# Optimization experiments

Measured on AMD Instinct MI355X. Metric: run time of the kernel, lower is better.

Reference implementation:

```python
import jax, jax.numpy as jnp
import numpy as np

NUM_HEADS = 12
DIM = 768
HEAD_DIM = DIM // NUM_HEADS
NUM_BUCKETS = 32
MAX_DISTANCE = 128
ELEV_SCALE = 1000.0


def _bucket_positions(relative_position):
    # Faithful port of RelativePositionBias2D._bucket_positions (torch .long() truncates;
    # values passed through the large branch are non-negative so astype(int32) matches).
    nb = NUM_BUCKETS // 2  # 16
    n = -relative_position
    ret = (n < 0).astype(jnp.int32) * nb
    n = jnp.abs(n)
    max_exact = nb // 2  # 8
    is_small = n < max_exact
    n_safe = jnp.maximum(n, 1).astype(jnp.float32)  # avoid log(0); masked by is_small
    val_if_large = max_exact + (
        jnp.log(n_safe / max_exact) / np.float32(np.log(MAX_DISTANCE / max_exact)) * (nb - max_exact)
    ).astype(jnp.int32)
    val_if_large = jnp.minimum(val_if_large, nb - 1)
    return ret + jnp.where(is_small, n, val_if_large)


def _bucket_idx(coords_2d):
    # coords_2d: [B, N, 2] in [0,1] -> integer grid coords
    coords_int = (coords_2d * MAX_DISTANCE).astype(jnp.int32)
    rel_x = coords_int[:, :, None, 0] - coords_int[:, None, :, 0]  # [B,N,N]
    rel_y = coords_int[:, :, None, 1] - coords_int[:, None, :, 1]
    bx = _bucket_positions(rel_x)
    by = _bucket_positions(rel_y)
    return bx * NUM_BUCKETS + by  # [B,N,N] int32 in [0, 1024)


def setup_inputs() -> dict:
    key = jax.random.key(0)
    ks = jax.random.split(key, 8)
    B, N, D = 4, 1024, DIM
    x = jax.random.normal(ks[0], (B, N, D), dtype=jnp.float32)
    coords_2d = jax.random.uniform(ks[1], (B, N, 2), dtype=jnp.float32)
    elevation_patches = jax.random.normal(ks[2], (B, N), dtype=jnp.float32) * 2000.0  # meters
    qkv_w = jax.random.normal(ks[3], (3 * D, D), dtype=jnp.float32) * 0.02
    qkv_b = jnp.zeros((3 * D,), dtype=jnp.float32)
    proj_w = jax.random.normal(ks[4], (D, D), dtype=jnp.float32) * 0.02
    proj_b = jnp.zeros((D,), dtype=jnp.float32)
    bias_table = jax.random.normal(ks[5], (NUM_BUCKETS * NUM_BUCKETS, NUM_HEADS), dtype=jnp.float32) * 0.02
    alpha = jnp.full((1,), 2.0, dtype=jnp.float32)
    return {"x": x, "coords_2d": coords_2d, "elevation_patches": elevation_patches,
            "qkv_w": qkv_w, "qkv_b": qkv_b, "proj_w": proj_w, "proj_b": proj_b,
            "bias_table": bias_table, "alpha": alpha}


def reference(x, coords_2d, elevation_patches, qkv_w, qkv_b, proj_w, proj_b, bias_table, alpha):
    B, N, D = x.shape
    H, hd = NUM_HEADS, HEAD_DIM
    scale = hd ** -0.5

    qkv = x @ qkv_w.T + qkv_b  # [B,N,3D]
    qkv = qkv.reshape(B, N, 3, H, hd)
    q = qkv[:, :, 0].transpose(0, 2, 1, 3)  # [B,H,N,hd]
    k = qkv[:, :, 1].transpose(0, 2, 1, 3)
    v = qkv[:, :, 2].transpose(0, 2, 1, 3)

    attn = jnp.einsum('bhnd,bhmd->bhnm', q * scale, k)  # [B,H,N,N]

    # relative position bias: gather from table, [B,N,N,H] -> [B,H,N,N]
    idx = _bucket_idx(coords_2d)
    rel_bias = bias_table[idx].transpose(0, 3, 1, 2)
    attn = attn + rel_bias

    # elevation bias: [B,N,N], broadcast over heads
    elev_diff = (elevation_patches[:, None, :] - elevation_patches[:, :, None]) / ELEV_SCALE
    elev_bias = jnp.clip(-alpha[0] * jax.nn.relu(elev_diff), -10.0, 0.0)
    attn = attn + elev_bias[:, None, :, :]

    attn = jax.nn.softmax(attn.astype(jnp.float32), axis=-1).astype(q.dtype)

    out = jnp.einsum('bhnm,bhmd->bhnd', attn, v)  # [B,H,N,hd]
    out = out.transpose(0, 2, 1, 3).reshape(B, N, D)
    return out @ proj_w.T + proj_b
```

## Files before the change

kernel.cpp:

```cpp
#include <hip/hip_runtime.h>
#include <hip/hip_bf16.h>
#include <math.h>

#define NH 12
#define HD 64
#define NSEQ 1024
#define DMODEL 768
#define LOG2E 1.44269504f

typedef unsigned short ushort_t;
typedef float f32x4 __attribute__((ext_vector_type(4)));
typedef short bf16x8 __attribute__((ext_vector_type(8)));

__device__ __forceinline__ ushort_t f2bf(float f) {
    unsigned int u = __float_as_uint(f);
    u += 0x7FFFu + ((u >> 16) & 1u);
    return (ushort_t)(u >> 16);
}

__device__ __forceinline__ unsigned pk2(float x, float y) {
    __hip_bfloat162 t = __float22bfloat162_rn(make_float2(x, y));
    union { __hip_bfloat162 b; unsigned u; } c; c.b = t;
    return c.u;
}

__device__ __forceinline__ void gl_lds16(const ushort_t* g, ushort_t* l) {
    __builtin_amdgcn_global_load_lds(
        (const __attribute__((address_space(1))) unsigned int*)g,
        (__attribute__((address_space(3))) unsigned int*)l, 16, 0, 0);
}

#define XB_N   3145728u
#define WQB_N  1769472u
#define PWB_N  589824u
#define CVT_BLOCKS 2400

__global__ __launch_bounds__(256) void prep_kernel(
    const float* __restrict__ x, const float* __restrict__ w1,
    ushort_t* __restrict__ dst)
{
    const int t = threadIdx.x;
    const unsigned i = blockIdx.x * 256 + t;
    const unsigned n0 = XB_N / 8, n1 = n0 + WQB_N / 8;
    if (i >= n1) return;
    const float* src; unsigned off;
    if (i < n0) { src = x;  off = i; }
    else        { src = w1; off = i - n0; }
    const float4 a = ((const float4*)src)[off * 2];
    const float4 b = ((const float4*)src)[off * 2 + 1];
    uint4 pk;
    pk.x = pk2(a.x, a.y); pk.y = pk2(a.z, a.w);
    pk.z = pk2(b.x, b.y); pk.w = pk2(b.z, b.w);
    ((uint4*)dst)[i] = pk;
}

__device__ __forceinline__ int bucketf(int rel) {
    const int n = -rel;
    const int u = (n < 0) ? 16 : 0;
    const int a = n < 0 ? -n : n;
    if (a < 8) return u + a;
    int v = 8 + (int)(log2f((float)a * 0.125f) * 2.0f + 1e-4f);
    if (v > 15) v = 15;
    return u + v;
}

#define QKV_BLOCKS 576
#define PACK_BLOCKS 4096
#define PW_BLOCKS 288

__global__ __launch_bounds__(256) void qkv_gemm(
    const ushort_t* __restrict__ A, const ushort_t* __restrict__ B,
    const float* __restrict__ bias,
    ushort_t* __restrict__ Qb, ushort_t* __restrict__ Kb, ushort_t* __restrict__ Vtb,
    const float* __restrict__ coords, const float* __restrict__ elev,
    const float* __restrict__ alpha_p, unsigned* __restrict__ pack,
    const float* __restrict__ pw, ushort_t* __restrict__ pwb)
{
    __shared__ __align__(16) ushort_t SM[32768];
    const int t = threadIdx.x;

    if (blockIdx.x >= QKV_BLOCKS + PACK_BLOCKS) {
        const unsigned i = (blockIdx.x - QKV_BLOCKS - PACK_BLOCKS) * 256 + t;
        if (i >= PWB_N / 8) return;
        const float4 a = ((const float4*)pw)[i * 2];
        const float4 b = ((const float4*)pw)[i * 2 + 1];
        uint4 pk;
        pk.x = pk2(a.x, a.y); pk.y = pk2(a.z, a.w);
        pk.z = pk2(b.x, b.y); pk.w = pk2(b.z, b.w);
        ((uint4*)pwb)[i] = pk;
        return;
    }
    if (blockIdx.x >= QKV_BLOCKS) {
        const int blk = blockIdx.x - QKV_BLOCKS;
        const int b = blk >> 10, i = blk & 1023;
        const float alpha = alpha_p[0];
        const float2 ci = *(const float2*)&coords[(size_t)(b * NSEQ + i) * 2];
        const int cxi = (int)(ci.x * 128.0f), cyi = (int)(ci.y * 128.0f);
        const float ei = elev[b * NSEQ + i];
        const int j0 = t * 4;
        const float4 c01 = *(const float4*)&coords[(size_t)(b * NSEQ + j0) * 2];
        const float4 c23 = *(const float4*)&coords[(size_t)(b * NSEQ + j0 + 2) * 2];
        const float4 ej4 = *(const float4*)&elev[b * NSEQ + j0];
        const float cjx[4] = {c01.x, c01.z, c23.x, c23.z};
        const float cjy[4] = {c01.y, c01.w, c23.y, c23.w};
        const float ejv[4] = {ej4.x, ej4.y, ej4.z, ej4.w};
        unsigned r[4];
        #pragma unroll
        for (int k = 0; k < 4; ++k) {
            const int bx = bucketf(cxi - (int)(cjx[k] * 128.0f));
            const int by = bucketf(cyi - (int)(cjy[k] * 128.0f));
            const int idx = (bx << 5) + by;
            const float ed = (ejv[k] - ei) * 1e-3f;
            const float eb = fmaxf(-alpha * fmaxf(ed, 0.0f), -10.0f) * LOG2E;
            r[k] = ((unsigned)f2bf(eb) << 16) | (unsigned)idx;
        }
        uint4 o; o.x = r[0]; o.y = r[1]; o.z = r[2]; o.w = r[3];
        *(uint4*)&pack[((size_t)b << 20) + (size_t)i * NSEQ + j0] = o;
        return;
    }

    const int lid = (blockIdx.x & 7) * 72 + (blockIdx.x >> 3);
    const int bx = lid % 18, by = lid / 18;
    const int m0 = by * 128, c0 = bx * 128;

    const int lane = t & 63, w = t >> 6;
    const int wr = w >> 1, wc = w & 1;
    const int col = lane & 15, quad = lane >> 4;
    const int c7 = col & 7;

    const f32x4 zero = {0.f, 0.f, 0.f, 0.f};
    f32x4 acc[4][4];
    #pragma unroll
    for (int i = 0; i < 4; ++i)
        #pragma unroll
        for (int j = 0; j < 4; ++j) acc[i][j] = zero;

    const int r8 = lane >> 3, g8 = lane & 7;
    const int gsw = ((g8 ^ r8) * 8);
    const ushort_t* Ag = A + (size_t)(m0 + w * 32 + r8) * DMODEL + gsw;
    const ushort_t* Bg = B + (size_t)(c0 + w * 32 + r8) * DMODEL + gsw;
    const int wso = (w * 32) * 64;

    auto STAGE = [&](int bo, int k0) {
        ushort_t* Aw = SM + bo + wso;
        ushort_t* Bw = SM + bo + 8192 + wso;
        gl_lds16(Ag + k0, Aw);
        gl_lds16(Ag + (size_t)8 * DMODEL + k0, Aw + 8 * 64);
        gl_lds16(Ag + (size_t)16 * DMODEL + k0, Aw + 16 * 64);
        gl_lds16(Ag + (size_t)24 * DMODEL + k0, Aw + 24 * 64);
        gl_lds16(Bg + k0, Bw);
        gl_lds16(Bg + (size_t)8 * DMODEL + k0, Bw + 8 * 64);
        gl_lds16(Bg + (size_t)16 * DMODEL + k0, Bw + 16 * 64);
        gl_lds16(Bg + (size_t)24 * DMODEL + k0, Bw + 24 * 64);
    };

    STAGE(0, 0);
    __syncthreads();

    #pragma unroll 2
    for (int k = 0; k < 12; ++k) {
        const int bo = (k & 1) * 16384;
        if (k < 11) STAGE(16384 - bo, (k + 1) * 64);
        #pragma unroll
        for (int kk = 0; kk < 2; ++kk) {
            bf16x8 af[4], bf[4];
            #pragma unroll
            for (int im = 0; im < 4; ++im)
                af[im] = *(const bf16x8*)&SM[bo + (wr * 64 + im * 16 + col) * 64
                        + ((4 * kk + quad) ^ c7) * 8];
            #pragma unroll
            for (int jn = 0; jn < 4; ++jn)
                bf[jn] = *(const bf16x8*)&SM[bo + 8192 + (wc * 64 + jn * 16 + col) * 64
                        + ((4 * kk + quad) ^ c7) * 8];
            #pragma unroll
            for (int im = 0; im < 4; ++im)
                #pragma unroll
                for (int jn = 0; jn < 4; ++jn)
                    acc[im][jn] = __builtin_amdgcn_mfma_f32_16x16x32_bf16(af[im], bf[jn], acc[im][jn], 0, 0, 0);
        }
        __syncthreads();
    }

    const int cbw = c0 + wc * 64;
    const int s = cbw / DMODEL;
    const int h = (cbw % DMODEL) >> 6;
    const int b = m0 >> 10;
    const int bh = b * NH + h;
    const int n0 = (m0 & (NSEQ - 1)) + wr * 64;

    float bv[4];
    #pragma unroll
    for (int jn = 0; jn < 4; ++jn) bv[jn] = bias[cbw + jn * 16 + col];

    if (s < 2) {
        ushort_t* lt = SM + w * 1152;
        ushort_t* dst = (s == 0) ? Qb : Kb;
        const float sc = (s == 0) ? 0.125f * LOG2E : 1.0f;
        const int row16 = lane >> 2, seg = lane & 3;
        #pragma unroll
        for (int im = 0; im < 4; ++im) {
            #pragma unroll
            for (int jn = 0; jn < 4; ++jn) {
                const f32x4 a = acc[im][jn];
                #pragma unroll
                for (int r = 0; r < 4; ++r)
                    lt[(quad * 4 + r) * 72 + jn * 16 + col] = f2bf((a[r] + bv[jn]) * sc);
            }
            const uint4 u0 = *(const uint4*)&lt[row16 * 72 + seg * 8];
            const uint4 u1 = *(const uint4*)&lt[row16 * 72 + 32 + seg * 8];
            const size_t gb = ((size_t)bh * NSEQ + n0 + im * 16 + row16) * HD
                            + seg * 8;
            *(uint4*)&dst[gb] = u0;
            *(uint4*)&dst[gb + 32] = u1;
        }
    } else {
        #pragma unroll
        for (int im = 0; im < 4; ++im) {
            #pragma unroll
            for (int jn = 0; jn < 4; ++jn) {
                const int d = jn * 16 + col;
                const float bvv = bv[jn];
                const f32x4 a = acc[im][jn];
                uint2 p;
                p.x = pk2(a[0] + bvv, a[1] + bvv);
                p.y = pk2(a[2] + bvv, a[3] + bvv);
                *(uint2*)&Vtb[((size_t)bh * HD + d) * NSEQ + n0 + im * 16 + quad * 4] = p;
            }
        }
    }
}

#define RBIAS(u) (__uint_as_float((unsigned)tabu[(u) & 1023u] << 16) \
                + __uint_as_float((u) & 0xFFFF0000u))

__global__ __launch_bounds__(256) void attn_mfma(
    const ushort_t* __restrict__ Qb, const ushort_t* __restrict__ Kb,
    const ushort_t* __restrict__ Vtb,
    const unsigned* __restrict__ pack,
    const float* __restrict__ table,
    ushort_t* __restrict__ Ob)
{
    __shared__ __align__(16) ushort_t Ks[2][64 * 72];
    __shared__ __align__(16) ushort_t Vt[2][64 * 72];
    __shared__ __align__(16) ushort_t Ps[64 * 72];
    __shared__ ushort_t tabu[1024];

    const int t = threadIdx.x;
    const int lane = t & 63, w = t >> 6;
    const int col = lane & 15, quad = lane >> 4;
    const int bid = (blockIdx.x & 7) * 96 + (blockIdx.x >> 3);
    const int it = bid & 15, bh = bid >> 4;
    const int h = bh % NH, b = bh / NH;
    const int i0 = it * 64;

    for (int i = t; i < 1024; i += 256)
        tabu[i] = f2bf(table[i * NH + h] * LOG2E);

    const ushort_t* Qg = Qb + ((size_t)bh * NSEQ + i0 + w * 16 + col) * HD;
    const bf16x8 aq0 = *(const bf16x8*)(Qg + quad * 8);
    const bf16x8 aq1 = *(const bf16x8*)(Qg + 32 + quad * 8);

    const size_t kvbase = (size_t)bh * NSEQ * HD;
    const unsigned* prow = pack + ((size_t)b << 20)
                         + (size_t)(i0 + w * 16 + col) * NSEQ + quad * 4;

    const int srow = t >> 3, sc8 = (t & 7) * 8;
    const int so0 = srow * 72 + sc8;
    const int so1 = (srow + 32) * 72 + sc8;

    uint4 k0 = *(const uint4*)&Kb[kvbase + (size_t)srow * HD + sc8];
    uint4 k1 = *(const uint4*)&Kb[kvbase + (size_t)(srow + 32) * HD + sc8];
    uint4 v0 = *(const uint4*)&Vtb[kvbase + (size_t)srow * NSEQ + sc8];
    uint4 v1 = *(const uint4*)&Vtb[kvbase + (size_t)(srow + 32) * NSEQ + sc8];
    *(uint4*)&Ks[0][so0] = k0;
    *(uint4*)&Ks[0][so1] = k1;
    *(uint4*)&Vt[0][so0] = v0;
    *(uint4*)&Vt[0][so1] = v1;
    k0 = *(const uint4*)&Kb[kvbase + (size_t)(64 + srow) * HD + sc8];
    k1 = *(const uint4*)&Kb[kvbase + (size_t)(64 + srow + 32) * HD + sc8];
    v0 = *(const uint4*)&Vtb[kvbase + (size_t)srow * NSEQ + 64 + sc8];
    v1 = *(const uint4*)&Vtb[kvbase + (size_t)(srow + 32) * NSEQ + 64 + sc8];

    uint4 pk4g[4], pk4l[4];
    #pragma unroll
    for (int jb = 0; jb < 4; ++jb)
        pk4g[jb] = *(const uint4*)(prow + jb * 16);

    __syncthreads();

    float rbc[4][4], rbn[4][4];
    #pragma unroll
    for (int jb = 0; jb < 4; ++jb) {
        const uint4 pkv = pk4g[jb];
        rbc[jb][0] = RBIAS(pkv.x);
        rbc[jb][1] = RBIAS(pkv.y);
        rbc[jb][2] = RBIAS(pkv.z);
        rbc[jb][3] = RBIAS(pkv.w);
    }
    #pragma unroll
    for (int jb = 0; jb < 4; ++jb)
        pk4g[jb] = *(const uint4*)(prow + 64 + jb * 16);

    const f32x4 zero = {0.f, 0.f, 0.f, 0.f};
    f32x4 o_acc[4];
    #pragma unroll
    for (int i = 0; i < 4; ++i) o_acc[i] = zero;
    float l_l = 0.f;

    #pragma unroll 2
    for (int jt = 0; jt < 16; ++jt) {
        __syncthreads();
        const int cur = jt & 1;

        if (jt < 15) {
            *(uint4*)&Ks[cur ^ 1][so0] = k0;
            *(uint4*)&Ks[cur ^ 1][so1] = k1;
            *(uint4*)&Vt[cur ^ 1][so0] = v0;
            *(uint4*)&Vt[cur ^ 1][so1] = v1;
        }
        if (jt < 14) {
            const int j2 = (jt + 2) * 64;
            k0 = *(const uint4*)&Kb[kvbase + (size_t)(j2 + srow) * HD + sc8];
            k1 = *(const uint4*)&Kb[kvbase + (size_t)(j2 + srow + 32) * HD + sc8];
            v0 = *(const uint4*)&Vtb[kvbase + (size_t)srow * NSEQ + j2 + sc8];
            v1 = *(const uint4*)&Vtb[kvbase + (size_t)(srow + 32) * NSEQ + j2 + sc8];
            #pragma unroll
            for (int jb = 0; jb < 4; ++jb)
                pk4l[jb] = *(const uint4*)(prow + j2 + jb * 16);
        }

        f32x4 sacc[4];
        __builtin_amdgcn_s_setprio(1);
        #pragma unroll
        for (int jb = 0; jb < 4; ++jb) {
            sacc[jb] = zero;
            const bf16x8 kb0 = *(const bf16x8*)&Ks[cur][(jb * 16 + col) * 72 + quad * 8];
            const bf16x8 kb1 = *(const bf16x8*)&Ks[cur][(jb * 16 + col) * 72 + 32 + quad * 8];
            sacc[jb] = __builtin_amdgcn_mfma_f32_16x16x32_bf16(kb0, aq0, sacc[jb], 0, 0, 0);
            sacc[jb] = __builtin_amdgcn_mfma_f32_16x16x32_bf16(kb1, aq1, sacc[jb], 0, 0, 0);
        }
        __builtin_amdgcn_s_setprio(0);

        float psum = 0.f;
        #pragma unroll
        for (int jb = 0; jb < 4; ++jb) {
            const float p0 = exp2f(sacc[jb][0] + rbc[jb][0]);
            const float p1 = exp2f(sacc[jb][1] + rbc[jb][1]);
            const float p2 = exp2f(sacc[jb][2] + rbc[jb][2]);
            const float p3 = exp2f(sacc[jb][3] + rbc[jb][3]);
            psum += (p0 + p1) + (p2 + p3);
            uint2 st;
            st.x = pk2(p0, p1);
            st.y = pk2(p2, p3);
            *(uint2*)&Ps[(w * 16 + col) * 72 + jb * 16 + quad * 4] = st;
        }
        l_l += psum;

        const bf16x8 ap0 = *(const bf16x8*)&Ps[(w * 16 + col) * 72 + quad * 8];
        const bf16x8 ap1 = *(const bf16x8*)&Ps[(w * 16 + col) * 72 + 32 + quad * 8];
        __builtin_amdgcn_s_setprio(1);
        #pragma unroll
        for (int db = 0; db < 4; ++db) {
            const bf16x8 vv0 = *(const bf16x8*)&Vt[cur][(db * 16 + col) * 72 + quad * 8];
            const bf16x8 vv1 = *(const bf16x8*)&Vt[cur][(db * 16 + col) * 72 + 32 + quad * 8];
            o_acc[db] = __builtin_amdgcn_mfma_f32_16x16x32_bf16(ap0, vv0, o_acc[db], 0, 0, 0);
            o_acc[db] = __builtin_amdgcn_mfma_f32_16x16x32_bf16(ap1, vv1, o_acc[db], 0, 0, 0);
            if (jt < 15) {
                const uint4 pkv = pk4g[db];
                rbn[db][0] = RBIAS(pkv.x);
                rbn[db][1] = RBIAS(pkv.y);
                rbn[db][2] = RBIAS(pkv.z);
                rbn[db][3] = RBIAS(pkv.w);
            }
        }
        __builtin_amdgcn_s_setprio(0);

        #pragma unroll
        for (int jb = 0; jb < 4; ++jb) {
            pk4g[jb] = pk4l[jb];
            rbc[jb][0] = rbn[jb][0];
            rbc[jb][1] = rbn[jb][1];
            rbc[jb][2] = rbn[jb][2];
            rbc[jb][3] = rbn[jb][3];
        }
    }

    float l = l_l;
    l += __shfl_xor(l, 16);
    l += __shfl_xor(l, 32);
    #pragma unroll
    for (int r = 0; r < 4; ++r) {
        const float lr = __shfl(l, w * 16 + quad * 4 + r);
        const float inv = 1.f / lr;
        const int ri = w * 16 + quad * 4 + r;
        const size_t base = ((size_t)(b * NSEQ) + i0 + ri) * DMODEL + h * HD;
        #pragma unroll
        for (int db = 0; db < 4; ++db)
            Ob[base + db * 16 + col] = f2bf(o_acc[db][r] * inv);
    }
}

__global__ __launch_bounds__(256) void proj_gemm(
    const ushort_t* __restrict__ A, const ushort_t* __restrict__ B,
    const float* __restrict__ bias, float* __restrict__ out)
{
    __shared__ __align__(16) ushort_t SM[16384];
    const int t = threadIdx.x;
    const int lane = t & 63, w = t >> 6;
    const int wr = w >> 1, wc = w & 1;
    const int col = lane & 15, quad = lane >> 4;
    const int c7 = col & 7;
    const int m0 = blockIdx.y * 64, c0 = blockIdx.x * 64;

    const f32x4 zero = {0.f, 0.f, 0.f, 0.f};
    f32x4 acc[2][2];
    #pragma unroll
    for (int i = 0; i < 2; ++i)
        #pragma unroll
        for (int j = 0; j < 2; ++j) acc[i][j] = zero;

    const int r8 = lane >> 3, g8 = lane & 7;
    const int gsw = ((g8 ^ r8) * 8);
    const ushort_t* Ag = A + (size_t)(m0 + w * 16 + r8) * DMODEL + gsw;
    const ushort_t* Bg = B + (size_t)(c0 + w * 16 + r8) * DMODEL + gsw;
    const int wso = (w * 16) * 64;

    auto STAGE = [&](int bo, int k0) {
        ushort_t* Aw = SM + bo + wso;
        ushort_t* Bw = SM + bo + 4096 + wso;
        gl_lds16(Ag + k0, Aw);
        gl_lds16(Ag + (size_t)8 * DMODEL + k0, Aw + 8 * 64);
        gl_lds16(Bg + k0, Bw);
        gl_lds16(Bg + (size_t)8 * DMODEL + k0, Bw + 8 * 64);
    };

    STAGE(0, 0);
    __syncthreads();

    #pragma unroll 2
    for (int k = 0; k < 12; ++k) {
        const int bo = (k & 1) * 8192;
        if (k < 11) STAGE(8192 - bo, (k + 1) * 64);
        #pragma unroll
        for (int kk = 0; kk < 2; ++kk) {
            bf16x8 af[2], bf[2];
            #pragma unroll
            for (int im = 0; im < 2; ++im)
                af[im] = *(const bf16x8*)&SM[bo + (wr * 32 + im * 16 + col) * 64
                        + ((4 * kk + quad) ^ c7) * 8];
            #pragma unroll
            for (int jn = 0; jn < 2; ++jn)
                bf[jn] = *(const bf16x8*)&SM[bo + 4096 + (wc * 32 + jn * 16 + col) * 64
                        + ((4 * kk + quad) ^ c7) * 8];
            #pragma unroll
            for (int im = 0; im < 2; ++im)
                #pragma unroll
                for (int jn = 0; jn < 2; ++jn)
                    acc[im][jn] = __builtin_amdgcn_mfma_f32_16x16x32_bf16(af[im], bf[jn], acc[im][jn], 0, 0, 0);
        }
        __syncthreads();
    }

    #pragma unroll
    for (int im = 0; im < 2; ++im) {
        #pragma unroll
        for (int jn = 0; jn < 2; ++jn) {
            const int c = c0 + wc * 32 + jn * 16 + col;
            const float bv = bias[c];
            #pragma unroll
            for (int r = 0; r < 4; ++r) {
                const int m = m0 + wr * 32 + im * 16 + quad * 4 + r;
                out[(size_t)m * DMODEL + c] = acc[im][jn][r] + bv;
            }
        }
    }
}

extern "C" void kernel_launch(void* const* d_in, const int* in_sizes, int n_in,
                              void* d_out, int out_size, void* d_ws, size_t ws_size,
                              hipStream_t stream) {
    const float* x       = (const float*)d_in[0];
    const float* coords  = (const float*)d_in[1];
    const float* elev    = (const float*)d_in[2];
    const float* qkv_w   = (const float*)d_in[3];
    const float* qkv_b   = (const float*)d_in[4];
    const float* proj_w  = (const float*)d_in[5];
    const float* proj_b  = (const float*)d_in[6];
    const float* btable  = (const float*)d_in[7];
    const float* alpha   = (const float*)d_in[8];
    float* out = (float*)d_out;

    ushort_t* wsu = (ushort_t*)d_ws;
    ushort_t* xb  = wsu;
    ushort_t* wqb = wsu + 3145728;
    ushort_t* pwb = wsu + 4915200;
    ushort_t* Qb  = wsu + 5505024;
    ushort_t* Kb  = wsu + 8650752;
    ushort_t* Vtb = wsu + 11796480;
    ushort_t* Ob  = wsu + 14942208;
    unsigned* pck = (unsigned*)(wsu + 18087936);

    prep_kernel<<<CVT_BLOCKS, 256, 0, stream>>>(x, qkv_w, wsu);
    qkv_gemm<<<QKV_BLOCKS + PACK_BLOCKS + PW_BLOCKS, 256, 0, stream>>>(
        xb, wqb, qkv_b, Qb, Kb, Vtb, coords, elev, alpha, pck, proj_w, pwb);
    attn_mfma<<<768, 256, 0, stream>>>(Qb, Kb, Vtb, pck, btable, Ob);
    proj_gemm<<<dim3(12, 64), 256, 0, stream>>>(Ob, pwb, proj_b, out);
}
```

Before: 168.3 us.

## Move bias packing and proj weight conversion into prep kernel, use bucket LUT

Moves the relative-position/elevation pack blocks and the proj_w bf16 conversion out of the QKV GEMM launch and into the prep kernel, so the GEMM kernel only launches its 576 tile blocks. The GEMM no longer carries the large shared-memory footprint for thousands of non-GEMM blocks. The bucket function is replaced by a 257-entry shared-memory lookup table per block, avoiding log2 per element. The cost is a block-level sync and LUT build in each pack block, and a bigger prep kernel that sits serially ahead of the GEMM.

```diff
diff --git a/kernel.cpp b/kernel.cpp
--- a/kernel.cpp
+++ b/kernel.cpp
@@ -33,26 +33,8 @@
 #define XB_N   3145728u
 #define WQB_N  1769472u
 #define PWB_N  589824u
-#define CVT_BLOCKS 2400
-
-__global__ __launch_bounds__(256) void prep_kernel(
-    const float* __restrict__ x, const float* __restrict__ w1,
-    ushort_t* __restrict__ dst)
-{
-    const int t = threadIdx.x;
-    const unsigned i = blockIdx.x * 256 + t;
-    const unsigned n0 = XB_N / 8, n1 = n0 + WQB_N / 8;
-    if (i >= n1) return;
-    const float* src; unsigned off;
-    if (i < n0) { src = x;  off = i; }
-    else        { src = w1; off = i - n0; }
-    const float4 a = ((const float4*)src)[off * 2];
-    const float4 b = ((const float4*)src)[off * 2 + 1];
-    uint4 pk;
-    pk.x = pk2(a.x, a.y); pk.y = pk2(a.z, a.w);
-    pk.z = pk2(b.x, b.y); pk.w = pk2(b.z, b.w);
-    ((uint4*)dst)[i] = pk;
-}
+#define CVT_BLOCKS 2688
+#define PACK_BLOCKS 4096
 
 __device__ __forceinline__ int bucketf(int rel) {
     const int n = -rel;
@@ -64,34 +46,34 @@
     return u + v;
 }
 
-#define QKV_BLOCKS 576
-#define PACK_BLOCKS 4096
-#define PW_BLOCKS 288
-
-__global__ __launch_bounds__(256) void qkv_gemm(
-    const ushort_t* __restrict__ A, const ushort_t* __restrict__ B,
-    const float* __restrict__ bias,
-    ushort_t* __restrict__ Qb, ushort_t* __restrict__ Kb, ushort_t* __restrict__ Vtb,
+__global__ __launch_bounds__(256) void prep_kernel(
+    const float* __restrict__ x, const float* __restrict__ w1,
+    const float* __restrict__ w2, ushort_t* __restrict__ dst,
     const float* __restrict__ coords, const float* __restrict__ elev,
-    const float* __restrict__ alpha_p, unsigned* __restrict__ pack,
-    const float* __restrict__ pw, ushort_t* __restrict__ pwb)
+    const float* __restrict__ alpha_p, unsigned* __restrict__ pack)
 {
-    __shared__ __align__(16) ushort_t SM[32768];
+    __shared__ unsigned char LUT[257];
     const int t = threadIdx.x;
-
-    if (blockIdx.x >= QKV_BLOCKS + PACK_BLOCKS) {
-        const unsigned i = (blockIdx.x - QKV_BLOCKS - PACK_BLOCKS) * 256 + t;
-        if (i >= PWB_N / 8) return;
-        const float4 a = ((const float4*)pw)[i * 2];
-        const float4 b = ((const float4*)pw)[i * 2 + 1];
+    if (blockIdx.x < CVT_BLOCKS) {
+        const unsigned i = blockIdx.x * 256 + t;
+        const unsigned n0 = XB_N / 8, n1 = n0 + WQB_N / 8, n2 = n1 + PWB_N / 8;
+        if (i >= n2) return;
+        const float* src; unsigned off;
+        if (i < n0)      { src = x;  off = i; }
+        else if (i < n1) { src = w1; off = i - n0; }
+        else             { src = w2; off = i - n1; }
+        const float4 a = ((const float4*)src)[off * 2];
+        const float4 b = ((const float4*)src)[off * 2 + 1];
         uint4 pk;
         pk.x = pk2(a.x, a.y); pk.y = pk2(a.z, a.w);
         pk.z = pk2(b.x, b.y); pk.w = pk2(b.z, b.w);
-        ((uint4*)pwb)[i] = pk;
-        return;
-    }
-    if (blockIdx.x >= QKV_BLOCKS) {
-        const int blk = blockIdx.x - QKV_BLOCKS;
+        ((uint4*)dst)[i] = pk;
+    } else {
+        LUT[t] = (unsigned char)bucketf(t - 128);
+        if (t == 0) LUT[256] = (unsigned char)bucketf(128);
+        __syncthreads();
+
+        const int blk = blockIdx.x - CVT_BLOCKS;
         const int b = blk >> 10, i = blk & 1023;
         const float alpha = alpha_p[0];
         const float2 ci = *(const float2*)&coords[(size_t)(b * NSEQ + i) * 2];
@@ -107,17 +89,27 @@
         unsigned r[4];
         #pragma unroll
         for (int k = 0; k < 4; ++k) {
-            const int bx = bucketf(cxi - (int)(cjx[k] * 128.0f));
-            const int by = bucketf(cyi - (int)(cjy[k] * 128.0f));
-            const int idx = (bx << 5) + by;
+            const int dx = cxi - (int)(cjx[k] * 128.0f);
+            const int dy = cyi - (int)(cjy[k] * 128.0f);
+            const int idx = ((int)LUT[dx + 128] << 5) | (int)LUT[dy + 128];
             const float ed = (ejv[k] - ei) * 1e-3f;
             const float eb = fmaxf(-alpha * fmaxf(ed, 0.0f), -10.0f) * LOG2E;
             r[k] = ((unsigned)f2bf(eb) << 16) | (unsigned)idx;
         }
         uint4 o; o.x = r[0]; o.y = r[1]; o.z = r[2]; o.w = r[3];
         *(uint4*)&pack[((size_t)b << 20) + (size_t)i * NSEQ + j0] = o;
-        return;
-    }
+    }
+}
+
+#define QKV_BLOCKS 576
+
+__global__ __launch_bounds__(256) void qkv_gemm(
+    const ushort_t* __restrict__ A, const ushort_t* __restrict__ B,
+    const float* __restrict__ bias,
+    ushort_t* __restrict__ Qb, ushort_t* __restrict__ Kb, ushort_t* __restrict__ Vtb)
+{
+    __shared__ __align__(16) ushort_t SM[32768];
+    const int t = threadIdx.x;
 
     const int lid = (blockIdx.x & 7) * 72 + (blockIdx.x >> 3);
     const int bx = lid % 18, by = lid / 18;
@@ -500,9 +492,9 @@
     ushort_t* Ob  = wsu + 14942208;
     unsigned* pck = (unsigned*)(wsu + 18087936);
 
-    prep_kernel<<<CVT_BLOCKS, 256, 0, stream>>>(x, qkv_w, wsu);
-    qkv_gemm<<<QKV_BLOCKS + PACK_BLOCKS + PW_BLOCKS, 256, 0, stream>>>(
-        xb, wqb, qkv_b, Qb, Kb, Vtb, coords, elev, alpha, pck, proj_w, pwb);
+    prep_kernel<<<CVT_BLOCKS + PACK_BLOCKS, 256, 0, stream>>>(
+        x, qkv_w, proj_w, wsu, coords, elev, alpha, pck);
+    qkv_gemm<<<QKV_BLOCKS, 256, 0, stream>>>(xb, wqb, qkv_b, Qb, Kb, Vtb);
     attn_mfma<<<768, 256, 0, stream>>>(Qb, Kb, Vtb, pck, btable, Ob);
     proj_gemm<<<dim3(12, 64), 256, 0, stream>>>(Ob, pwb, proj_b, out);
 }
```

After: 170.1 us. No clear change (+1.1%).
